# Optimization experiments

Measured on AMD Instinct MI355X. Metric: run time of the kernel, lower is better.

## Reference

```python
import jax, jax.numpy as jnp
import numpy as np
from jax import lax


def setup_inputs() -> dict:
    key = jax.random.key(0)
    k1, k2, k3, k4, k5 = jax.random.split(key, 5)
    B, Cin, Cout, H, W, K, S = 16, 256, 256, 128, 128, 3, 512
    x = jax.random.normal(k1, (B, Cin, H, W), dtype=jnp.float32)
    style = jax.random.normal(k2, (B, S), dtype=jnp.float32)
    # parameters (kaiming-ish scales)
    conv_w = jax.random.normal(k3, (Cout, Cin, K, K), dtype=jnp.float32) * (1.0 / np.sqrt(Cin * K * K))
    fc_w = jax.random.normal(k4, (Cout, S), dtype=jnp.float32) * (1.0 / np.sqrt(S))
    fc_b = jax.random.normal(k5, (Cout,), dtype=jnp.float32) * 0.01
    return {"x": x, "style": style, "conv_w": conv_w, "fc_w": fc_w, "fc_b": fc_b}


def reference(x, style, conv_w, fc_w, fc_b):
    # style_fc: (B, S) @ (S, Cout) + b -> per-sample per-output-channel scale
    s = style @ fc_w.T + fc_b  # (B, Cout)
    # Modulating W[o] by s[b,o] on the output-channel axis commutes with the
    # convolution, so the per-sample loop is a single conv + channel scale.
    # (Original uses F.conv2d with bias=None, so conv bias is never applied.)
    y = lax.conv_general_dilated(
        x, conv_w,
        window_strides=(1, 1),
        padding=[(1, 1), (1, 1)],
        dimension_numbers=("NCHW", "OIHW", "NCHW"),
    )  # (B, Cout, H, W)
    return y * s[:, :, None, None]
```

## Files before the change

kernel.cpp:

```cpp
#include <hip/hip_runtime.h>
#include <stdint.h>

typedef __attribute__((ext_vector_type(8))) short bf16x8;
typedef __attribute__((ext_vector_type(8))) unsigned short u16x8;
typedef __attribute__((ext_vector_type(4))) float f32x4;

#define NB   16
#define CIN  256
#define COUT 256
#define HH   128
#define WW   128
#define SDIM 512

#define KPAD 72
#define NCOL 130
#define BHALF (3 * NCOL * KPAD)
#define B_BYTES (BHALF * 2)
#define LDS_BYTES (2 * B_BYTES + COUT * 4)

__device__ __forceinline__ unsigned short f2bf(float f) {
    unsigned int u = __float_as_uint(f);
    u += 0x7fff + ((u >> 16) & 1);
    return (unsigned short)(u >> 16);
}

__global__ void style_fc_kernel(const float* __restrict__ style,
                                const float* __restrict__ fc_w,
                                const float* __restrict__ fc_b,
                                float* __restrict__ s_out) {
    const int b = blockIdx.x;
    const int co = threadIdx.x;
    const f32x4* st = (const f32x4*)(style + b * SDIM);
    const f32x4* w  = (const f32x4*)(fc_w + co * SDIM);
    float acc = fc_b[co];
    #pragma unroll 4
    for (int k = 0; k < SDIM / 4; ++k) {
        f32x4 a = st[k], c = w[k];
        acc += a.x * c.x + a.y * c.y + a.z * c.z + a.w * c.w;
    }
    s_out[b * COUT + co] = acc;
}

__global__ void wt_transform_kernel(const float* __restrict__ conv_w,
                                    unsigned short* __restrict__ wt) {
    __shared__ unsigned short T[9][256];
    const int co = blockIdx.x;
    const int ci = threadIdx.x;
    const float* src = conv_w + ((size_t)co * CIN + ci) * 9;
    float v[9];
    #pragma unroll
    for (int t = 0; t < 9; ++t) v[t] = src[t];
    #pragma unroll
    for (int t = 0; t < 9; ++t) T[t][ci] = f2bf(v[t]);
    __syncthreads();
    const unsigned int* T32 = (const unsigned int*)&T[0][0];
    unsigned int* out32 = (unsigned int*)wt;
    for (int idx = ci; idx < 1152; idx += 256) {
        const int d = idx & 31;
        const int r = idx >> 5;
        out32[(((size_t)r * COUT + co) << 5) + d] = T32[idx];
    }
}

__global__ void __launch_bounds__(512, 2)
modconv_kernel(const float* __restrict__ x,
               const unsigned short* __restrict__ wt,
               const float* __restrict__ s,
               float* __restrict__ out) {
    extern __shared__ char lds[];
    unsigned short* B0 = (unsigned short*)lds;
    unsigned short* B1 = B0 + BHALF;
    float* Sl = (float*)(lds + 2 * B_BYTES);

    const int tid  = threadIdx.x;
    const int lane = tid & 63;
    const int wid  = tid >> 6;
    const int bid  = blockIdx.x;
    const int nid  = (bid & 7) * 256 + (bid >> 3);
    const int bb   = nid >> 7;
    const int h    = nid & 127;

    {
        f32x4 z = {0.f, 0.f, 0.f, 0.f};
        for (int i = tid; i < (2 * B_BYTES) / 16; i += 512)
            *(f32x4*)(lds + i * 16) = z;
    }
    if (tid < COUT) Sl[tid] = s[bb * COUT + tid];

    f32x4 acc[4][4];
    {
        f32x4 z = {0.f, 0.f, 0.f, 0.f};
        #pragma unroll
        for (int mi = 0; mi < 4; ++mi)
            #pragma unroll
            for (int nj = 0; nj < 4; ++nj)
                acc[mi][nj] = z;
    }

    const int wm = wid >> 1;
    const int wn = wid & 1;
    const int cobase = wm * 64;
    const int wbase  = wn * 64;
    const int l15 = lane & 15;
    const int kl8 = (lane >> 4) * 8;
    const int g   = wid;

    float xv[3][2][8];

    auto LOADX = [&](int q) {
        #pragma unroll
        for (int kh = 0; kh < 3; ++kh) {
            const int r = h + kh - 1;
            if (r >= 0 && r < HH) {
                const float* xs = x + (((size_t)(bb * CIN + q * 64 + g * 8)) * HH + r) * WW;
                #pragma unroll
                for (int half = 0; half < 2; ++half)
                    #pragma unroll
                    for (int j = 0; j < 8; ++j)
                        xv[kh][half][j] = xs[j * (HH * WW) + lane + half * 64];
            } else {
                #pragma unroll
                for (int half = 0; half < 2; ++half)
                    #pragma unroll
                    for (int j = 0; j < 8; ++j)
                        xv[kh][half][j] = 0.0f;
            }
        }
    };
    auto WRITEX = [&](unsigned short* Bd) {
        #pragma unroll
        for (int kh = 0; kh < 3; ++kh)
            #pragma unroll
            for (int half = 0; half < 2; ++half) {
                u16x8 vv;
                #pragma unroll
                for (int j = 0; j < 8; ++j) vv[j] = f2bf(xv[kh][half][j]);
                *(u16x8*)(Bd + (kh * NCOL + 1 + lane + half * 64) * KPAD + g * 8) = vv;
            }
    };
    auto LOADA = [&](bf16x8* a, int q, int t, int kk) {
        const unsigned short* p = wt + (((size_t)(t * 4 + q) * COUT + cobase + l15) << 6) + kk + kl8;
        #pragma unroll
        for (int mi = 0; mi < 4; ++mi)
            a[mi] = *(const bf16x8*)(p + (mi << 10));
    };
    auto LOADB = [&](bf16x8* b, const unsigned short* Bc, int kh, int kw, int kk) {
        #pragma unroll
        for (int nj = 0; nj < 4; ++nj)
            b[nj] = *(const bf16x8*)(Bc + (kh * NCOL + wbase + nj * 16 + l15 + kw) * KPAD + kk + kl8);
    };

    __syncthreads();
    LOADX(0);
    WRITEX(B0);
    __syncthreads();

    bf16x8 aA[4], aB[4];
    LOADA(aA, 0, 0, 0);

    #pragma unroll 1
    for (int q = 0; q < 4; ++q) {
        unsigned short* Bc = (q & 1) ? B1 : B0;
        unsigned short* Bn = (q & 1) ? B0 : B1;
        if (q < 3) LOADX(q + 1);
        const int qn = (q < 3) ? q + 1 : 3;

        #pragma unroll
        for (int t = 0; t < 9; ++t) {
            const int kh = t / 3;
            const int kw = t - kh * 3;
            bf16x8 b[4];
            LOADB(b, Bc, kh, kw, 0);
            LOADA(aB, q, t, 32);
            #pragma unroll
            for (int mi = 0; mi < 4; ++mi)
                #pragma unroll
                for (int nj = 0; nj < 4; ++nj)
                    acc[mi][nj] = __builtin_amdgcn_mfma_f32_16x16x32_bf16(
                        aA[mi], b[nj], acc[mi][nj], 0, 0, 0);
            LOADB(b, Bc, kh, kw, 32);
            if (t < 8) LOADA(aA, q, t + 1, 0);
            else       LOADA(aA, qn, 0, 0);
            #pragma unroll
            for (int mi = 0; mi < 4; ++mi)
                #pragma unroll
                for (int nj = 0; nj < 4; ++nj)
                    acc[mi][nj] = __builtin_amdgcn_mfma_f32_16x16x32_bf16(
                        aB[mi], b[nj], acc[mi][nj], 0, 0, 0);
        }

        if (q < 3) {
            WRITEX(Bn);
            __syncthreads();
        }
    }

    const int rowD = (lane >> 4) * 4;
    #pragma unroll
    for (int mi = 0; mi < 4; ++mi) {
        #pragma unroll
        for (int r = 0; r < 4; ++r) {
            const int co = cobase + mi * 16 + rowD + r;
            const float sv = Sl[co];
            float* orow = out + (((size_t)(bb * COUT + co) * HH + h) * WW);
            #pragma unroll
            for (int nj = 0; nj < 4; ++nj)
                orow[wbase + nj * 16 + l15] = acc[mi][nj][r] * sv;
        }
    }
}

extern "C" void kernel_launch(void* const* d_in, const int* in_sizes, int n_in,
                              void* d_out, int out_size, void* d_ws, size_t ws_size,
                              hipStream_t stream) {
    const float* x      = (const float*)d_in[0];
    const float* style  = (const float*)d_in[1];
    const float* conv_w = (const float*)d_in[2];
    const float* fc_w   = (const float*)d_in[3];
    const float* fc_b   = (const float*)d_in[4];
    float* out = (float*)d_out;

    float* s_ws = (float*)d_ws;
    unsigned short* wt = (unsigned short*)((char*)d_ws + 16384);

    hipFuncSetAttribute(reinterpret_cast<const void*>(modconv_kernel),
                        hipFuncAttributeMaxDynamicSharedMemorySize, LDS_BYTES);

    style_fc_kernel<<<NB, COUT, 0, stream>>>(style, fc_w, fc_b, s_ws);
    wt_transform_kernel<<<COUT, 256, 0, stream>>>(conv_w, wt);
    modconv_kernel<<<NB * HH, 512, LDS_BYTES, stream>>>(x, wt, s_ws, out);
}
```

Before: 956.4 us.

## Double block to 16 waves with 64x32 per-wave output tiles

Launches the conv kernel with 1024 threads, splitting the 128-wide row across four waves instead of two so each wave computes a 64x32 tile with half the accumulators. x staging is redistributed so each thread loads one column. This cuts register pressure and raises wave count for latency hiding. In exchange it halves MFMA work per weight fragment load, doubling global weight traffic per output.

```diff
diff --git a/kernel.cpp b/kernel.cpp
--- a/kernel.cpp
+++ b/kernel.cpp
@@ -17,6 +17,7 @@
 #define BHALF (3 * NCOL * KPAD)
 #define B_BYTES (BHALF * 2)
 #define LDS_BYTES (2 * B_BYTES + COUT * 4)
+#define NTHR 1024
 
 __device__ __forceinline__ unsigned short f2bf(float f) {
     unsigned int u = __float_as_uint(f);
@@ -62,7 +63,7 @@
     }
 }
 
-__global__ void __launch_bounds__(512, 2)
+__global__ void __launch_bounds__(NTHR, 4)
 modconv_kernel(const float* __restrict__ x,
                const unsigned short* __restrict__ wt,
                const float* __restrict__ s,
@@ -82,61 +83,56 @@
 
     {
         f32x4 z = {0.f, 0.f, 0.f, 0.f};
-        for (int i = tid; i < (2 * B_BYTES) / 16; i += 512)
+        for (int i = tid; i < (2 * B_BYTES) / 16; i += NTHR)
             *(f32x4*)(lds + i * 16) = z;
     }
     if (tid < COUT) Sl[tid] = s[bb * COUT + tid];
 
-    f32x4 acc[4][4];
+    f32x4 acc[4][2];
     {
         f32x4 z = {0.f, 0.f, 0.f, 0.f};
         #pragma unroll
         for (int mi = 0; mi < 4; ++mi)
             #pragma unroll
-            for (int nj = 0; nj < 4; ++nj)
+            for (int nj = 0; nj < 2; ++nj)
                 acc[mi][nj] = z;
     }
 
-    const int wm = wid >> 1;
-    const int wn = wid & 1;
+    const int wm = wid >> 2;
+    const int wn = wid & 3;
     const int cobase = wm * 64;
-    const int wbase  = wn * 64;
+    const int wbase  = wn * 32;
     const int l15 = lane & 15;
     const int kl8 = (lane >> 4) * 8;
-    const int g   = wid;
-
-    float xv[3][2][8];
+    const int g   = tid >> 7;
+    const int c   = tid & 127;
+
+    float xv[3][8];
 
     auto LOADX = [&](int q) {
         #pragma unroll
         for (int kh = 0; kh < 3; ++kh) {
             const int r = h + kh - 1;
             if (r >= 0 && r < HH) {
-                const float* xs = x + (((size_t)(bb * CIN + q * 64 + g * 8)) * HH + r) * WW;
-                #pragma unroll
-                for (int half = 0; half < 2; ++half)
-                    #pragma unroll
-                    for (int j = 0; j < 8; ++j)
-                        xv[kh][half][j] = xs[j * (HH * WW) + lane + half * 64];
+                const float* xs = x + (((size_t)(bb * CIN + q * 64 + g * 8)) * HH + r) * WW + c;
+                #pragma unroll
+                for (int j = 0; j < 8; ++j)
+                    xv[kh][j] = xs[j * (HH * WW)];
             } else {
                 #pragma unroll
-                for (int half = 0; half < 2; ++half)
-                    #pragma unroll
-                    for (int j = 0; j < 8; ++j)
-                        xv[kh][half][j] = 0.0f;
+                for (int j = 0; j < 8; ++j)
+                    xv[kh][j] = 0.0f;
             }
         }
     };
     auto WRITEX = [&](unsigned short* Bd) {
         #pragma unroll
-        for (int kh = 0; kh < 3; ++kh)
-            #pragma unroll
-            for (int half = 0; half < 2; ++half) {
-                u16x8 vv;
-                #pragma unroll
-                for (int j = 0; j < 8; ++j) vv[j] = f2bf(xv[kh][half][j]);
-                *(u16x8*)(Bd + (kh * NCOL + 1 + lane + half * 64) * KPAD + g * 8) = vv;
-            }
+        for (int kh = 0; kh < 3; ++kh) {
+            u16x8 vv;
+            #pragma unroll
+            for (int j = 0; j < 8; ++j) vv[j] = f2bf(xv[kh][j]);
+            *(u16x8*)(Bd + (kh * NCOL + 1 + c) * KPAD + g * 8) = vv;
+        }
     };
     auto LOADA = [&](bf16x8* a, int q, int t, int kk) {
         const unsigned short* p = wt + (((size_t)(t * 4 + q) * COUT + cobase + l15) << 6) + kk + kl8;
@@ -146,7 +142,7 @@
     };
     auto LOADB = [&](bf16x8* b, const unsigned short* Bc, int kh, int kw, int kk) {
         #pragma unroll
-        for (int nj = 0; nj < 4; ++nj)
+        for (int nj = 0; nj < 2; ++nj)
             b[nj] = *(const bf16x8*)(Bc + (kh * NCOL + wbase + nj * 16 + l15 + kw) * KPAD + kk + kl8);
     };
 
@@ -169,13 +165,13 @@
         for (int t = 0; t < 9; ++t) {
             const int kh = t / 3;
             const int kw = t - kh * 3;
-            bf16x8 b[4];
+            bf16x8 b[2];
             LOADB(b, Bc, kh, kw, 0);
             LOADA(aB, q, t, 32);
             #pragma unroll
             for (int mi = 0; mi < 4; ++mi)
                 #pragma unroll
-                for (int nj = 0; nj < 4; ++nj)
+                for (int nj = 0; nj < 2; ++nj)
                     acc[mi][nj] = __builtin_amdgcn_mfma_f32_16x16x32_bf16(
                         aA[mi], b[nj], acc[mi][nj], 0, 0, 0);
             LOADB(b, Bc, kh, kw, 32);
@@ -184,7 +180,7 @@
             #pragma unroll
             for (int mi = 0; mi < 4; ++mi)
                 #pragma unroll
-                for (int nj = 0; nj < 4; ++nj)
+                for (int nj = 0; nj < 2; ++nj)
                     acc[mi][nj] = __builtin_amdgcn_mfma_f32_16x16x32_bf16(
                         aB[mi], b[nj], acc[mi][nj], 0, 0, 0);
         }
@@ -204,7 +200,7 @@
             const float sv = Sl[co];
             float* orow = out + (((size_t)(bb * COUT + co) * HH + h) * WW);
             #pragma unroll
-            for (int nj = 0; nj < 4; ++nj)
+            for (int nj = 0; nj < 2; ++nj)
                 orow[wbase + nj * 16 + l15] = acc[mi][nj][r] * sv;
         }
     }
@@ -228,5 +224,5 @@
 
     style_fc_kernel<<<NB, COUT, 0, stream>>>(style, fc_w, fc_b, s_ws);
     wt_transform_kernel<<<COUT, 256, 0, stream>>>(conv_w, wt);
-    modconv_kernel<<<NB * HH, 512, LDS_BYTES, stream>>>(x, wt, s_ws, out);
-}
+    modconv_kernel<<<NB * HH, NTHR, LDS_BYTES, stream>>>(x, wt, s_ws, out);
+}
```

Result: slower. 1.447 ms (+51.3%).

## Compute two output rows per block, reusing weights and staged input rows

Applied to the files above, without the earlier changes.

Each block now produces two output rows instead of one. It stages four input rows into one LDS buffer, so every weight fragment loaded from global memory feeds twice as many MFMAs and the grid is halved. The register-prefetched double buffer is replaced by a single buffer that is loaded synchronously between barriers, which drops the overlap of x loads with compute. Accumulator registers double to 128 floats per thread, which may cut occupancy under the launch bounds of 512 threads and 2 blocks.

```diff
diff --git a/kernel.cpp b/kernel.cpp
--- a/kernel.cpp
+++ b/kernel.cpp
@@ -14,9 +14,10 @@
 
 #define KPAD 72
 #define NCOL 130
-#define BHALF (3 * NCOL * KPAD)
-#define B_BYTES (BHALF * 2)
-#define LDS_BYTES (2 * B_BYTES + COUT * 4)
+#define BROWS 4
+#define B_BYTES (BROWS * NCOL * KPAD * 2)
+#define LDS_BYTES (B_BYTES + COUT * 4)
+#define NBLK (NB * (HH / 2))
 
 __device__ __forceinline__ unsigned short f2bf(float f) {
     unsigned int u = __float_as_uint(f);
@@ -68,33 +69,34 @@
                const float* __restrict__ s,
                float* __restrict__ out) {
     extern __shared__ char lds[];
-    unsigned short* B0 = (unsigned short*)lds;
-    unsigned short* B1 = B0 + BHALF;
-    float* Sl = (float*)(lds + 2 * B_BYTES);
+    unsigned short* Bl = (unsigned short*)lds;
+    float* Sl = (float*)(lds + B_BYTES);
 
     const int tid  = threadIdx.x;
     const int lane = tid & 63;
     const int wid  = tid >> 6;
     const int bid  = blockIdx.x;
-    const int nid  = (bid & 7) * 256 + (bid >> 3);
-    const int bb   = nid >> 7;
-    const int h    = nid & 127;
+    const int nid  = (bid & 7) * (NBLK / 8) + (bid >> 3);
+    const int bb   = nid >> 6;
+    const int h0   = (nid & 63) * 2;
 
     {
         f32x4 z = {0.f, 0.f, 0.f, 0.f};
-        for (int i = tid; i < (2 * B_BYTES) / 16; i += 512)
+        for (int i = tid; i < B_BYTES / 16; i += 512)
             *(f32x4*)(lds + i * 16) = z;
     }
     if (tid < COUT) Sl[tid] = s[bb * COUT + tid];
 
-    f32x4 acc[4][4];
+    f32x4 acc[4][4][2];
     {
         f32x4 z = {0.f, 0.f, 0.f, 0.f};
         #pragma unroll
         for (int mi = 0; mi < 4; ++mi)
             #pragma unroll
             for (int nj = 0; nj < 4; ++nj)
-                acc[mi][nj] = z;
+                #pragma unroll
+                for (int hh = 0; hh < 2; ++hh)
+                    acc[mi][nj][hh] = z;
     }
 
     const int wm = wid >> 1;
@@ -103,56 +105,43 @@
     const int wbase  = wn * 64;
     const int l15 = lane & 15;
     const int kl8 = (lane >> 4) * 8;
-    const int g   = wid;
-
-    float xv[3][2][8];
-
-    auto LOADX = [&](int q) {
-        #pragma unroll
-        for (int kh = 0; kh < 3; ++kh) {
-            const int r = h + kh - 1;
+    const int p  = tid >> 7;
+    const int c  = tid & 127;
+
+    auto STAGE = [&](int q) {
+        #pragma unroll
+        for (int rr = 0; rr < BROWS; ++rr) {
+            const int r = h0 - 1 + rr;
             if (r >= 0 && r < HH) {
-                const float* xs = x + (((size_t)(bb * CIN + q * 64 + g * 8)) * HH + r) * WW;
-                #pragma unroll
-                for (int half = 0; half < 2; ++half)
+                #pragma unroll
+                for (int jj = 0; jj < 2; ++jj) {
+                    const int o = p + jj * 4;
+                    const float* xs = x + (((size_t)(bb * CIN + q * 64 + o * 8)) * HH + r) * WW + c;
+                    u16x8 vv;
                     #pragma unroll
                     for (int j = 0; j < 8; ++j)
-                        xv[kh][half][j] = xs[j * (HH * WW) + lane + half * 64];
-            } else {
-                #pragma unroll
-                for (int half = 0; half < 2; ++half)
-                    #pragma unroll
-                    for (int j = 0; j < 8; ++j)
-                        xv[kh][half][j] = 0.0f;
+                        vv[j] = f2bf(xs[j * (HH * WW)]);
+                    *(u16x8*)(Bl + (rr * NCOL + 1 + c) * KPAD + o * 8) = vv;
+                }
             }
         }
-    };
-    auto WRITEX = [&](unsigned short* Bd) {
-        #pragma unroll
-        for (int kh = 0; kh < 3; ++kh)
-            #pragma unroll
-            for (int half = 0; half < 2; ++half) {
-                u16x8 vv;
-                #pragma unroll
-                for (int j = 0; j < 8; ++j) vv[j] = f2bf(xv[kh][half][j]);
-                *(u16x8*)(Bd + (kh * NCOL + 1 + lane + half * 64) * KPAD + g * 8) = vv;
-            }
     };
     auto LOADA = [&](bf16x8* a, int q, int t, int kk) {
-        const unsigned short* p = wt + (((size_t)(t * 4 + q) * COUT + cobase + l15) << 6) + kk + kl8;
+        const unsigned short* ptr = wt + (((size_t)(t * 4 + q) * COUT + cobase + l15) << 6) + kk + kl8;
         #pragma unroll
         for (int mi = 0; mi < 4; ++mi)
-            a[mi] = *(const bf16x8*)(p + (mi << 10));
+            a[mi] = *(const bf16x8*)(ptr + (mi << 10));
     };
-    auto LOADB = [&](bf16x8* b, const unsigned short* Bc, int kh, int kw, int kk) {
-        #pragma unroll
-        for (int nj = 0; nj < 4; ++nj)
-            b[nj] = *(const bf16x8*)(Bc + (kh * NCOL + wbase + nj * 16 + l15 + kw) * KPAD + kk + kl8);
+    auto LOADB8 = [&](bf16x8* b, int kh, int kw, int kk) {
+        #pragma unroll
+        for (int hh = 0; hh < 2; ++hh)
+            #pragma unroll
+            for (int nj = 0; nj < 4; ++nj)
+                b[hh * 4 + nj] = *(const bf16x8*)(Bl + ((kh + hh) * NCOL + wbase + nj * 16 + l15 + kw) * KPAD + kk + kl8);
     };
 
     __syncthreads();
-    LOADX(0);
-    WRITEX(B0);
+    STAGE(0);
     __syncthreads();
 
     bf16x8 aA[4], aB[4];
@@ -160,37 +149,37 @@
 
     #pragma unroll 1
     for (int q = 0; q < 4; ++q) {
-        unsigned short* Bc = (q & 1) ? B1 : B0;
-        unsigned short* Bn = (q & 1) ? B0 : B1;
-        if (q < 3) LOADX(q + 1);
         const int qn = (q < 3) ? q + 1 : 3;
-
         #pragma unroll
         for (int t = 0; t < 9; ++t) {
             const int kh = t / 3;
             const int kw = t - kh * 3;
-            bf16x8 b[4];
-            LOADB(b, Bc, kh, kw, 0);
+            bf16x8 b[8];
+            LOADB8(b, kh, kw, 0);
             LOADA(aB, q, t, 32);
             #pragma unroll
             for (int mi = 0; mi < 4; ++mi)
                 #pragma unroll
-                for (int nj = 0; nj < 4; ++nj)
-                    acc[mi][nj] = __builtin_amdgcn_mfma_f32_16x16x32_bf16(
-                        aA[mi], b[nj], acc[mi][nj], 0, 0, 0);
-            LOADB(b, Bc, kh, kw, 32);
+                for (int hh = 0; hh < 2; ++hh)
+                    #pragma unroll
+                    for (int nj = 0; nj < 4; ++nj)
+                        acc[mi][nj][hh] = __builtin_amdgcn_mfma_f32_16x16x32_bf16(
+                            aA[mi], b[hh * 4 + nj], acc[mi][nj][hh], 0, 0, 0);
+            LOADB8(b, kh, kw, 32);
             if (t < 8) LOADA(aA, q, t + 1, 0);
             else       LOADA(aA, qn, 0, 0);
             #pragma unroll
             for (int mi = 0; mi < 4; ++mi)
                 #pragma unroll
-                for (int nj = 0; nj < 4; ++nj)
-                    acc[mi][nj] = __builtin_amdgcn_mfma_f32_16x16x32_bf16(
-                        aB[mi], b[nj], acc[mi][nj], 0, 0, 0);
-        }
-
+                for (int hh = 0; hh < 2; ++hh)
+                    #pragma unroll
+                    for (int nj = 0; nj < 4; ++nj)
+                        acc[mi][nj][hh] = __builtin_amdgcn_mfma_f32_16x16x32_bf16(
+                            aB[mi], b[hh * 4 + nj], acc[mi][nj][hh], 0, 0, 0);
+        }
         if (q < 3) {
-            WRITEX(Bn);
+            __syncthreads();
+            STAGE(q + 1);
             __syncthreads();
         }
     }
@@ -202,10 +191,13 @@
         for (int r = 0; r < 4; ++r) {
             const int co = cobase + mi * 16 + rowD + r;
             const float sv = Sl[co];
-            float* orow = out + (((size_t)(bb * COUT + co) * HH + h) * WW);
-            #pragma unroll
-            for (int nj = 0; nj < 4; ++nj)
-                orow[wbase + nj * 16 + l15] = acc[mi][nj][r] * sv;
+            #pragma unroll
+            for (int hh = 0; hh < 2; ++hh) {
+                float* orow = out + (((size_t)(bb * COUT + co) * HH + h0 + hh) * WW);
+                #pragma unroll
+                for (int nj = 0; nj < 4; ++nj)
+                    orow[wbase + nj * 16 + l15] = acc[mi][nj][hh][r] * sv;
+            }
         }
     }
 }
@@ -228,5 +220,5 @@
 
     style_fc_kernel<<<NB, COUT, 0, stream>>>(style, fc_w, fc_b, s_ws);
     wt_transform_kernel<<<COUT, 256, 0, stream>>>(conv_w, wt);
-    modconv_kernel<<<NB * HH, 512, LDS_BYTES, stream>>>(x, wt, s_ws, out);
-}
+    modconv_kernel<<<NBLK, 512, LDS_BYTES, stream>>>(x, wt, s_ws, out);
+}
```

Result: faster. 843.8 us (-11.8%).
